# Performance work log

Hardware: AMD Instinct MI355X
Metric: run time of the kernel (lower is better)

## Reference

```python
import jax, jax.numpy as jnp
import numpy as np

B, S, D = 4, 4096, 128

def setup_inputs() -> dict:
    key = jax.random.key(0)
    kq, kk, kv = jax.random.split(key, 3)
    q = jax.random.normal(kq, (B, S, D), dtype=jnp.float32)
    k = jax.random.normal(kk, (B, S, D), dtype=jnp.float32)
    v = jax.random.normal(kv, (B, S, D), dtype=jnp.float32)
    return {"q": q, "k": k, "v": v}

def reference(q, k, v):
    d_model = q.shape[-1]
    scale = 1.0 / jnp.sqrt(jnp.asarray(d_model, q.dtype))
    # [B, S, S] scores
    scores = jnp.einsum('bqd,bkd->bqk', q, k) * scale
    s = q.shape[1]
    causal = jnp.tril(jnp.ones((s, s), dtype=bool))
    neg_inf = jnp.asarray(-jnp.inf, scores.dtype)
    scores = jnp.where(causal[None, :, :], scores, neg_inf)
    attn = jax.nn.softmax(scores, axis=-1)
    return jnp.einsum('bqk,bkd->bqd', attn, v)
```

## Files before the change

### kernel.cpp

```cpp
#include <hip/hip_runtime.h>


#define B_   4
#define S_   4096
#define D_   128
#define BN   64
#define NT_  64
#define QT_  32
#define NCHB 119
#define BLOB_SHORTS 16384
#define MASKVAL (-1.0e30f)
#define DEFER_THR 8.0f

typedef __attribute__((ext_vector_type(8))) short bf16x8;
typedef __attribute__((ext_vector_type(4))) float f32x4;

__device__ __host__ __forceinline__ constexpr int chunks_of(int t) { return (2 * t + 11) / 10; }
constexpr int nchb_calc() { int s = 0; for (int t = 0; t < QT_; ++t) s += chunks_of(t); return s; }
static_assert(nchb_calc() == NCHB, "chunk count mismatch");

__device__ __forceinline__ short f2bf(float x) {
    unsigned u = __builtin_bit_cast(unsigned, x);
    unsigned r = (u + 0x7fffu + ((u >> 16) & 1u)) >> 16;
    return (short)r;
}
__device__ __forceinline__ float ex2(float x) { return __builtin_amdgcn_exp2f(x); }
__device__ __forceinline__ unsigned cvtpk(float lo, float hi) {
    unsigned r;
    asm("v_cvt_pk_bf16_f32 %0, %1, %2" : "=v"(r) : "v"(lo), "v"(hi));
    return r;
}
__device__ __forceinline__ void gl_lds16(const short* g, short* l) {
    __builtin_amdgcn_global_load_lds(
        (const __attribute__((address_space(1))) unsigned int*)g,
        (__attribute__((address_space(3))) unsigned int*)l, 16, 0, 0);
}

__global__ __launch_bounds__(256) void prep(const float* __restrict__ Qg,
                                            const float* __restrict__ Kg,
                                            const float* __restrict__ Vg,
                                            short* __restrict__ Qbf,
                                            short* __restrict__ KV)
{
    __shared__ short vt[64][40];
    const int id  = blockIdx.x;
    const int tid = threadIdx.x;
    const float SC = 0.12751740f;

    if (id < 1024) {
        const int b = id & 3, tile = (id >> 2) & 63, q4 = id >> 8;
        const int n = q4 * 16 + (tid >> 4);
        const int G = tid & 15;
        const size_t rowoff = ((size_t)b * S_ + (size_t)tile * 64 + n) * D_ + G * 8;
        short* blob = KV + (size_t)(b * NT_ + tile) * BLOB_SHORTS;
        {
            float4 a = *reinterpret_cast<const float4*>(Qg + rowoff);
            float4 c = *reinterpret_cast<const float4*>(Qg + rowoff + 4);
            bf16x8 v;
            v[0] = f2bf(a.x * SC); v[1] = f2bf(a.y * SC); v[2] = f2bf(a.z * SC); v[3] = f2bf(a.w * SC);
            v[4] = f2bf(c.x * SC); v[5] = f2bf(c.y * SC); v[6] = f2bf(c.z * SC); v[7] = f2bf(c.w * SC);
            *reinterpret_cast<bf16x8*>(Qbf + rowoff) = v;
        }
        {
            float4 a = *reinterpret_cast<const float4*>(Kg + rowoff);
            float4 c = *reinterpret_cast<const float4*>(Kg + rowoff + 4);
            bf16x8 v;
            v[0] = f2bf(a.x); v[1] = f2bf(a.y); v[2] = f2bf(a.z); v[3] = f2bf(a.w);
            v[4] = f2bf(c.x); v[5] = f2bf(c.y); v[6] = f2bf(c.z); v[7] = f2bf(c.w);
            const int p = (G & 8) | ((G & 7) ^ (n & 7));
            *reinterpret_cast<bf16x8*>(blob + n * 128 + p * 8) = v;
        }
    } else {
        const int u = id - 1024;
        const int b = u & 3, tile = (u >> 2) & 63, dq = u >> 8;
        short* blob = KV + (size_t)(b * NT_ + tile) * BLOB_SHORTS;
        {
            const int n = tid >> 2, c8 = tid & 3;
            const size_t off = ((size_t)b * S_ + (size_t)tile * 64 + n) * D_ + dq * 32 + c8 * 8;
            float4 a = *reinterpret_cast<const float4*>(Vg + off);
            float4 c = *reinterpret_cast<const float4*>(Vg + off + 4);
            bf16x8 v;
            v[0] = f2bf(a.x); v[1] = f2bf(a.y); v[2] = f2bf(a.z); v[3] = f2bf(a.w);
            v[4] = f2bf(c.x); v[5] = f2bf(c.y); v[6] = f2bf(c.z); v[7] = f2bf(c.w);
            *reinterpret_cast<bf16x8*>(&vt[n][c8 * 8]) = v;
        }
        __syncthreads();
        {
            const int dl = tid >> 3, G = tid & 7;
            const int d  = dq * 32 + dl;
            bf16x8 g;
#pragma unroll
            for (int i = 0; i < 8; ++i) g[i] = vt[G * 8 + i][dl];
            const int p = G ^ (d & 7);
            *reinterpret_cast<bf16x8*>(blob + 8192 + d * 64 + p * 8) = g;
        }
    }
}

template<bool SPLIT>
__global__ __launch_bounds__(512, 4) void fa_fwd(const short* __restrict__ Qbf,
                                                 const short* __restrict__ KV,
                                                 float* __restrict__ Og,
                                                 unsigned* __restrict__ Op,
                                                 float* __restrict__ Ml)
{
    __shared__ short lkv[2][BLOB_SHORTS];
    __shared__ unsigned pbuf[8][256];

    const int tid  = threadIdx.x;
    const int wv   = tid >> 6;
    const int lane = tid & 63;
    const int m    = lane & 15;
    const int quad = lane >> 4;
    const int m7   = m & 7;

    int batch, t, lo, hi, chunk_id;
    {
        const int id = blockIdx.x;
        batch = id & 3;
        int u = id >> 2;
        if (SPLIT) {
            int tt = QT_ - 1, base = 0, rt;
            for (;;) { rt = chunks_of(tt); if (u < base + rt) break; base += rt; --tt; }
            t = tt;
            const int r  = u - base;
            const int nk = 2 * t + 2;
            lo = r * nk / rt;
            hi = (r + 1) * nk / rt;
            chunk_id = batch * NCHB + u;
        } else {
            t  = QT_ - 1 - u;
            lo = 0; hi = 2 * t + 2; chunk_id = 0;
        }
        if (lo >= hi) return;
    }

    bf16x8 qf[4];
    {
        const short* qp = Qbf + ((size_t)batch * S_ + (size_t)t * 128 + wv * 16 + m) * D_ + quad * 8;
#pragma unroll
        for (int c = 0; c < 4; ++c)
            qf[c] = *reinterpret_cast<const bf16x8*>(qp + c * 32);
    }

    f32x4 acc[8];
#pragma unroll
    for (int i = 0; i < 8; ++i) acc[i] = (f32x4){0.f, 0.f, 0.f, 0.f};
    float mrun = MASKVAL, lrun = 0.f;

    const size_t tilebase = (size_t)batch * NT_ * BLOB_SHORTS;
    const int qtop = t * 128 + wv * 16 + 15;
#define STAGE(KT, BUF) do {                                                   \
        const short* g_ = KV + tilebase + (size_t)(KT) * BLOB_SHORTS + tid * 8;\
        short* l_ = (BUF) + tid * 8;                                          \
        _Pragma("unroll")                                                     \
        for (int c_ = 0; c_ < 4; ++c_)                                        \
            gl_lds16(g_ + c_ * 4096, l_ + c_ * 4096);                         \
    } while (0)

    STAGE(lo, lkv[0]);

    for (int kt = lo; kt < hi; ++kt) {
        const short* cur = lkv[(kt - lo) & 1];
        short* nxt = lkv[(kt - lo + 1) & 1];
        __syncthreads();
        if (kt + 1 < hi) STAGE(kt + 1, nxt);

        if (kt * 64 > qtop) continue;

        const short* lk = cur;
        const short* lv = cur + 8192;

        f32x4 st[4];
#pragma unroll
        for (int nt = 0; nt < 4; ++nt) st[nt] = (f32x4){0.f, 0.f, 0.f, 0.f};
        __builtin_amdgcn_s_setprio(1);
#pragma unroll
        for (int c = 0; c < 4; ++c) {
            const int p = ((c >> 1) * 8) | ((((c & 1) * 4) | quad) ^ m7);
#pragma unroll
            for (int nt = 0; nt < 4; ++nt) {
                bf16x8 kf = *reinterpret_cast<const bf16x8*>(lk + nt * 2048 + m * 128 + p * 8);
                st[nt] = __builtin_amdgcn_mfma_f32_16x16x32_bf16(kf, qf[c], st[nt], 0, 0, 0);
            }
        }
        __builtin_amdgcn_s_setprio(0);

        if (kt >= 2 * t) {
            const int kbase = (kt - 2 * t) * 64;
            const int qloc  = wv * 16 + m;
#pragma unroll
            for (int nt = 0; nt < 4; ++nt)
#pragma unroll
                for (int r = 0; r < 4; ++r)
                    if (kbase + nt * 16 + quad * 4 + r > qloc) st[nt][r] = MASKVAL;
        }

        float t0 = fmaxf(fmaxf(st[0][0], st[0][1]), fmaxf(st[0][2], st[0][3]));
        float t1 = fmaxf(fmaxf(st[1][0], st[1][1]), fmaxf(st[1][2], st[1][3]));
        float t2 = fmaxf(fmaxf(st[2][0], st[2][1]), fmaxf(st[2][2], st[2][3]));
        float t3 = fmaxf(fmaxf(st[3][0], st[3][1]), fmaxf(st[3][2], st[3][3]));
        float mx = fmaxf(fmaxf(t0, t1), fmaxf(t2, t3));
        if (__any(mx - mrun > DEFER_THR)) {
            float mw = fmaxf(mx, __shfl_xor(mx, 16));
            mw = fmaxf(mw, __shfl_xor(mw, 32));
            const float mnew = fmaxf(mrun, mw);
            const float al   = ex2(mrun - mnew);
            mrun = mnew;
            lrun *= al;
#pragma unroll
            for (int r = 0; r < 4; ++r) {
                float alq = __shfl(al, quad * 4 + r);
#pragma unroll
                for (int ct = 0; ct < 8; ++ct) acc[ct][r] *= alq;
            }
        }
        float sum = 0.f;
#pragma unroll
        for (int nt = 0; nt < 4; ++nt)
#pragma unroll
            for (int r = 0; r < 4; ++r) {
                float pv = ex2(st[nt][r] - mrun);
                st[nt][r] = pv;
                sum += pv;
            }
        lrun += sum;

        {
            unsigned* pb = &pbuf[wv][0];
            const int swz = (m & 3) << 2;
#pragma unroll
            for (int ks = 0; ks < 2; ++ks) {
#pragma unroll
                for (int h = 0; h < 2; ++h) {
                    const int nt = 2 * ks + h;
                    uint2 w;
                    w.x = cvtpk(st[nt][0], st[nt][1]);
                    w.y = cvtpk(st[nt][2], st[nt][3]);
                    *reinterpret_cast<uint2*>(pb + m * 16 + ((h * 8 + quad * 2) ^ swz)) = w;
                }
                uint4 wi = *reinterpret_cast<const uint4*>(pb + m * 16 + ((quad * 4) ^ swz));
                bf16x8 pf = __builtin_bit_cast(bf16x8, wi);
                const int p = (ks * 4 + quad) ^ m7;
                __builtin_amdgcn_s_setprio(1);
#pragma unroll
                for (int ct = 0; ct < 8; ++ct) {
                    bf16x8 vf = *reinterpret_cast<const bf16x8*>(lv + ct * 1024 + m * 64 + p * 8);
                    acc[ct] = __builtin_amdgcn_mfma_f32_16x16x32_bf16(pf, vf, acc[ct], 0, 0, 0);
                }
                __builtin_amdgcn_s_setprio(0);
            }
        }
    }
#undef STAGE

    lrun += __shfl_xor(lrun, 16);
    lrun += __shfl_xor(lrun, 32);

    const int row0 = wv * 16 + quad * 4;
    if (SPLIT) {
        unsigned* ob = Op + (size_t)chunk_id * (128 * 64);
#pragma unroll
        for (int r = 0; r < 4; ++r) {
            uint4 w;
            w.x = cvtpk(acc[0][r], acc[1][r]);
            w.y = cvtpk(acc[2][r], acc[3][r]);
            w.z = cvtpk(acc[4][r], acc[5][r]);
            w.w = cvtpk(acc[6][r], acc[7][r]);
            *reinterpret_cast<uint4*>(ob + (row0 + r) * 64 + m * 4) = w;
        }
        if (lane < 16) {
            float* mlb = Ml + (size_t)chunk_id * (128 * 2) + (wv * 16 + lane) * 2;
            mlb[0] = mrun;
            mlb[1] = lrun;
        }
    } else {
        const float inv = 1.0f / lrun;
        const size_t obase = ((size_t)batch * S_ + (size_t)t * 128 + row0) * D_;
#pragma unroll
        for (int r = 0; r < 4; ++r) {
            float invq = __shfl(inv, quad * 4 + r);
#pragma unroll
            for (int ct = 0; ct < 8; ++ct)
                Og[obase + (size_t)r * D_ + ct * 16 + m] = acc[ct][r] * invq;
        }
    }
}

__global__ __launch_bounds__(256) void fa_merge(const unsigned* __restrict__ Op,
                                                const float* __restrict__ Ml,
                                                float* __restrict__ Og)
{
    const int x   = blockIdx.x;
    const int btq = x >> 4;
    const int oct = x & 15;
    const int t   = btq & (QT_ - 1);
    const int b   = btq >> 5;
    const int rt  = chunks_of(t);
    int base = 0;
    for (int tt = QT_ - 1; tt > t; --tt) base += chunks_of(tt);
    const int cbase = b * NCHB + base;
    const int row = oct * 8 + (threadIdx.x >> 5);
    const int g   = threadIdx.x & 31;

    float mr_[7], lr_[7];
    float mg = MASKVAL;
#pragma unroll
    for (int r = 0; r < 7; ++r)
        if (r < rt) {
            float2 ml2 = *reinterpret_cast<const float2*>(
                Ml + (size_t)(cbase + r) * (128 * 2) + row * 2);
            mr_[r] = ml2.x;
            lr_[r] = ml2.y;
            mg = fmaxf(mg, mr_[r]);
        }
    float l = 0.f;
    float a0 = 0.f, a1 = 0.f, a2 = 0.f, a3 = 0.f;
#pragma unroll
    for (int r = 0; r < 7; ++r)
        if (r < rt) {
            float w = ex2(mr_[r] - mg);
            l += lr_[r] * w;
            uint2 pk = *reinterpret_cast<const uint2*>(
                Op + (size_t)(cbase + r) * (128 * 64) + row * 64 + g * 2);
            a0 += w * __builtin_bit_cast(float, pk.x << 16);
            a1 += w * __builtin_bit_cast(float, pk.x & 0xffff0000u);
            a2 += w * __builtin_bit_cast(float, pk.y << 16);
            a3 += w * __builtin_bit_cast(float, pk.y & 0xffff0000u);
        }
    const float inv = 1.0f / l;
    float* og = Og + (size_t)btq * (128 * D_) + row * D_;
    const int d0 = 64 * (g & 1) + (g >> 1);
    og[d0]      = a0 * inv;
    og[d0 + 16] = a1 * inv;
    og[d0 + 32] = a2 * inv;
    og[d0 + 48] = a3 * inv;
}

extern "C" void kernel_launch(void* const* d_in, const int* in_sizes, int n_in,
                              void* d_out, int out_size, void* d_ws, size_t ws_size,
                              hipStream_t stream) {
    const float* q = (const float*)d_in[0];
    const float* k = (const float*)d_in[1];
    const float* v = (const float*)d_in[2];
    float* o = (float*)d_out;

    const size_t QBF_BYTES = (size_t)B_ * S_ * D_ * 2;
    const size_t KV_BYTES  = (size_t)B_ * NT_ * BLOB_SHORTS * 2;
    const size_t PREFIX    = QBF_BYTES + KV_BYTES;
    const int    NCH       = B_ * NCHB;
    const size_t O_BYTES   = (size_t)NCH * 128 * 64 * 4;
    const size_t ML_BYTES  = (size_t)NCH * 128 * 2 * 4;
    const size_t NEEDED    = PREFIX + O_BYTES + ML_BYTES;

    char* ws = (char*)d_ws;
    short* Qbf = (short*)ws;
    short* KV  = (short*)(ws + QBF_BYTES);

    prep<<<dim3(2048), 256, 0, stream>>>(q, k, v, Qbf, KV);

    if (ws_size >= NEEDED) {
        unsigned* Op = (unsigned*)(ws + PREFIX);
        float* Ml = (float*)(ws + PREFIX + O_BYTES);
        fa_fwd<true><<<dim3(NCH), 512, 0, stream>>>(Qbf, KV, nullptr, Op, Ml);
        fa_merge<<<dim3(B_ * QT_ * 16), 256, 0, stream>>>(Op, Ml, o);
    } else {
        fa_fwd<false><<<dim3(B_ * QT_), 512, 0, stream>>>(Qbf, KV, o, nullptr, nullptr);
    }
}
```

Before: 112.7 us.

## Give each wave two 16-row query tiles and halve block size to 256 threads

Each wavefront now handles 32 query rows as two 16-row halves, reusing every K and V fragment read from LDS for two MFMAs. The block shrinks from 8 to 4 waves, with the K/V staging loop doubled to cover the same tile. This halves LDS read traffic per MFMA but doubles accumulator and score register use per thread and cuts waves per block, which may lower occupancy and latency hiding.

Result: no change. 113.0 us (+0.3%).

```diff
diff --git a/kernel.cpp b/kernel.cpp
--- a/kernel.cpp
+++ b/kernel.cpp
@@ -98,14 +98,14 @@
 }
 
 template<bool SPLIT>
-__global__ __launch_bounds__(512, 4) void fa_fwd(const short* __restrict__ Qbf,
+__global__ __launch_bounds__(256, 2) void fa_fwd(const short* __restrict__ Qbf,
                                                  const short* __restrict__ KV,
                                                  float* __restrict__ Og,
                                                  unsigned* __restrict__ Op,
                                                  float* __restrict__ Ml)
 {
     __shared__ short lkv[2][BLOB_SHORTS];
-    __shared__ unsigned pbuf[8][256];
+    __shared__ unsigned pbuf[4][512];
 
     const int tid  = threadIdx.x;
     const int wv   = tid >> 6;
@@ -135,27 +135,31 @@
         if (lo >= hi) return;
     }
 
-    bf16x8 qf[4];
-    {
-        const short* qp = Qbf + ((size_t)batch * S_ + (size_t)t * 128 + wv * 16 + m) * D_ + quad * 8;
+    bf16x8 qf[2][4];
+#pragma unroll
+    for (int qh = 0; qh < 2; ++qh) {
+        const short* qp = Qbf + ((size_t)batch * S_ + (size_t)t * 128 + wv * 32 + qh * 16 + m) * D_ + quad * 8;
 #pragma unroll
         for (int c = 0; c < 4; ++c)
-            qf[c] = *reinterpret_cast<const bf16x8*>(qp + c * 32);
-    }
-
-    f32x4 acc[8];
-#pragma unroll
-    for (int i = 0; i < 8; ++i) acc[i] = (f32x4){0.f, 0.f, 0.f, 0.f};
-    float mrun = MASKVAL, lrun = 0.f;
+            qf[qh][c] = *reinterpret_cast<const bf16x8*>(qp + c * 32);
+    }
+
+    f32x4 acc[2][8];
+#pragma unroll
+    for (int qh = 0; qh < 2; ++qh)
+#pragma unroll
+        for (int i = 0; i < 8; ++i) acc[qh][i] = (f32x4){0.f, 0.f, 0.f, 0.f};
+    float mrun[2] = {MASKVAL, MASKVAL};
+    float lrun[2] = {0.f, 0.f};
 
     const size_t tilebase = (size_t)batch * NT_ * BLOB_SHORTS;
-    const int qtop = t * 128 + wv * 16 + 15;
+    const int qtop = t * 128 + wv * 32 + 31;
 #define STAGE(KT, BUF) do {                                                   \
         const short* g_ = KV + tilebase + (size_t)(KT) * BLOB_SHORTS + tid * 8;\
         short* l_ = (BUF) + tid * 8;                                          \
         _Pragma("unroll")                                                     \
-        for (int c_ = 0; c_ < 4; ++c_)                                        \
-            gl_lds16(g_ + c_ * 4096, l_ + c_ * 4096);                         \
+        for (int c_ = 0; c_ < 8; ++c_)                                        \
+            gl_lds16(g_ + c_ * 2048, l_ + c_ * 2048);                         \
     } while (0)
 
     STAGE(lo, lkv[0]);
@@ -171,9 +175,11 @@
         const short* lk = cur;
         const short* lv = cur + 8192;
 
-        f32x4 st[4];
-#pragma unroll
-        for (int nt = 0; nt < 4; ++nt) st[nt] = (f32x4){0.f, 0.f, 0.f, 0.f};
+        f32x4 st[2][4];
+#pragma unroll
+        for (int qh = 0; qh < 2; ++qh)
+#pragma unroll
+            for (int nt = 0; nt < 4; ++nt) st[qh][nt] = (f32x4){0.f, 0.f, 0.f, 0.f};
         __builtin_amdgcn_s_setprio(1);
 #pragma unroll
         for (int c = 0; c < 4; ++c) {
@@ -181,72 +187,85 @@
 #pragma unroll
             for (int nt = 0; nt < 4; ++nt) {
                 bf16x8 kf = *reinterpret_cast<const bf16x8*>(lk + nt * 2048 + m * 128 + p * 8);
-                st[nt] = __builtin_amdgcn_mfma_f32_16x16x32_bf16(kf, qf[c], st[nt], 0, 0, 0);
+                st[0][nt] = __builtin_amdgcn_mfma_f32_16x16x32_bf16(kf, qf[0][c], st[0][nt], 0, 0, 0);
+                st[1][nt] = __builtin_amdgcn_mfma_f32_16x16x32_bf16(kf, qf[1][c], st[1][nt], 0, 0, 0);
             }
         }
         __builtin_amdgcn_s_setprio(0);
 
         if (kt >= 2 * t) {
             const int kbase = (kt - 2 * t) * 64;
-            const int qloc  = wv * 16 + m;
+#pragma unroll
+            for (int qh = 0; qh < 2; ++qh) {
+                const int qloc = wv * 32 + qh * 16 + m;
+#pragma unroll
+                for (int nt = 0; nt < 4; ++nt)
+#pragma unroll
+                    for (int r = 0; r < 4; ++r)
+                        if (kbase + nt * 16 + quad * 4 + r > qloc) st[qh][nt][r] = MASKVAL;
+            }
+        }
+
+#pragma unroll
+        for (int qh = 0; qh < 2; ++qh) {
+            float t0 = fmaxf(fmaxf(st[qh][0][0], st[qh][0][1]), fmaxf(st[qh][0][2], st[qh][0][3]));
+            float t1 = fmaxf(fmaxf(st[qh][1][0], st[qh][1][1]), fmaxf(st[qh][1][2], st[qh][1][3]));
+            float t2 = fmaxf(fmaxf(st[qh][2][0], st[qh][2][1]), fmaxf(st[qh][2][2], st[qh][2][3]));
+            float t3 = fmaxf(fmaxf(st[qh][3][0], st[qh][3][1]), fmaxf(st[qh][3][2], st[qh][3][3]));
+            float mx = fmaxf(fmaxf(t0, t1), fmaxf(t2, t3));
+            if (__any(mx - mrun[qh] > DEFER_THR)) {
+                float mw = fmaxf(mx, __shfl_xor(mx, 16));
+                mw = fmaxf(mw, __shfl_xor(mw, 32));
+                const float mnew = fmaxf(mrun[qh], mw);
+                const float al   = ex2(mrun[qh] - mnew);
+                mrun[qh] = mnew;
+                lrun[qh] *= al;
+#pragma unroll
+                for (int r = 0; r < 4; ++r) {
+                    float alq = __shfl(al, quad * 4 + r);
+#pragma unroll
+                    for (int ct = 0; ct < 8; ++ct) acc[qh][ct][r] *= alq;
+                }
+            }
+            float sum = 0.f;
 #pragma unroll
             for (int nt = 0; nt < 4; ++nt)
 #pragma unroll
-                for (int r = 0; r < 4; ++r)
-                    if (kbase + nt * 16 + quad * 4 + r > qloc) st[nt][r] = MASKVAL;
-        }
-
-        float t0 = fmaxf(fmaxf(st[0][0], st[0][1]), fmaxf(st[0][2], st[0][3]));
-        float t1 = fmaxf(fmaxf(st[1][0], st[1][1]), fmaxf(st[1][2], st[1][3]));
-        float t2 = fmaxf(fmaxf(st[2][0], st[2][1]), fmaxf(st[2][2], st[2][3]));
-        float t3 = fmaxf(fmaxf(st[3][0], st[3][1]), fmaxf(st[3][2], st[3][3]));
-        float mx = fmaxf(fmaxf(t0, t1), fmaxf(t2, t3));
-        if (__any(mx - mrun > DEFER_THR)) {
-            float mw = fmaxf(mx, __shfl_xor(mx, 16));
-            mw = fmaxf(mw, __shfl_xor(mw, 32));
-            const float mnew = fmaxf(mrun, mw);
-            const float al   = ex2(mrun - mnew);
-            mrun = mnew;
-            lrun *= al;
-#pragma unroll
-            for (int r = 0; r < 4; ++r) {
-                float alq = __shfl(al, quad * 4 + r);
-#pragma unroll
-                for (int ct = 0; ct < 8; ++ct) acc[ct][r] *= alq;
-            }
-        }
-        float sum = 0.f;
-#pragma unroll
-        for (int nt = 0; nt < 4; ++nt)
-#pragma unroll
-            for (int r = 0; r < 4; ++r) {
-                float pv = ex2(st[nt][r] - mrun);
-                st[nt][r] = pv;
-                sum += pv;
-            }
-        lrun += sum;
+                for (int r = 0; r < 4; ++r) {
+                    float pv = ex2(st[qh][nt][r] - mrun[qh]);
+                    st[qh][nt][r] = pv;
+                    sum += pv;
+                }
+            lrun[qh] += sum;
+        }
 
         {
-            unsigned* pb = &pbuf[wv][0];
             const int swz = (m & 3) << 2;
 #pragma unroll
             for (int ks = 0; ks < 2; ++ks) {
 #pragma unroll
-                for (int h = 0; h < 2; ++h) {
-                    const int nt = 2 * ks + h;
-                    uint2 w;
-                    w.x = cvtpk(st[nt][0], st[nt][1]);
-                    w.y = cvtpk(st[nt][2], st[nt][3]);
-                    *reinterpret_cast<uint2*>(pb + m * 16 + ((h * 8 + quad * 2) ^ swz)) = w;
+                for (int qh = 0; qh < 2; ++qh) {
+                    unsigned* pb = &pbuf[wv][qh * 256];
+#pragma unroll
+                    for (int h = 0; h < 2; ++h) {
+                        const int nt = 2 * ks + h;
+                        uint2 w;
+                        w.x = cvtpk(st[qh][nt][0], st[qh][nt][1]);
+                        w.y = cvtpk(st[qh][nt][2], st[qh][nt][3]);
+                        *reinterpret_cast<uint2*>(pb + m * 16 + ((h * 8 + quad * 2) ^ swz)) = w;
+                    }
                 }
-                uint4 wi = *reinterpret_cast<const uint4*>(pb + m * 16 + ((quad * 4) ^ swz));
-                bf16x8 pf = __builtin_bit_cast(bf16x8, wi);
+                uint4 wi0 = *reinterpret_cast<const uint4*>(&pbuf[wv][0]   + m * 16 + ((quad * 4) ^ swz));
+                uint4 wi1 = *reinterpret_cast<const uint4*>(&pbuf[wv][256] + m * 16 + ((quad * 4) ^ swz));
+                bf16x8 pf0 = __builtin_bit_cast(bf16x8, wi0);
+                bf16x8 pf1 = __builtin_bit_cast(bf16x8, wi1);
                 const int p = (ks * 4 + quad) ^ m7;
                 __builtin_amdgcn_s_setprio(1);
 #pragma unroll
                 for (int ct = 0; ct < 8; ++ct) {
                     bf16x8 vf = *reinterpret_cast<const bf16x8*>(lv + ct * 1024 + m * 64 + p * 8);
-                    acc[ct] = __builtin_amdgcn_mfma_f32_16x16x32_bf16(pf, vf, acc[ct], 0, 0, 0);
+                    acc[0][ct] = __builtin_amdgcn_mfma_f32_16x16x32_bf16(pf0, vf, acc[0][ct], 0, 0, 0);
+                    acc[1][ct] = __builtin_amdgcn_mfma_f32_16x16x32_bf16(pf1, vf, acc[1][ct], 0, 0, 0);
                 }
                 __builtin_amdgcn_s_setprio(0);
             }
@@ -254,35 +273,48 @@
     }
 #undef STAGE
 
-    lrun += __shfl_xor(lrun, 16);
-    lrun += __shfl_xor(lrun, 32);
-
-    const int row0 = wv * 16 + quad * 4;
+#pragma unroll
+    for (int qh = 0; qh < 2; ++qh) {
+        lrun[qh] += __shfl_xor(lrun[qh], 16);
+        lrun[qh] += __shfl_xor(lrun[qh], 32);
+    }
+
     if (SPLIT) {
         unsigned* ob = Op + (size_t)chunk_id * (128 * 64);
 #pragma unroll
-        for (int r = 0; r < 4; ++r) {
-            uint4 w;
-            w.x = cvtpk(acc[0][r], acc[1][r]);
-            w.y = cvtpk(acc[2][r], acc[3][r]);
-            w.z = cvtpk(acc[4][r], acc[5][r]);
-            w.w = cvtpk(acc[6][r], acc[7][r]);
-            *reinterpret_cast<uint4*>(ob + (row0 + r) * 64 + m * 4) = w;
+        for (int qh = 0; qh < 2; ++qh) {
+            const int row0 = wv * 32 + qh * 16 + quad * 4;
+#pragma unroll
+            for (int r = 0; r < 4; ++r) {
+                uint4 w;
+                w.x = cvtpk(acc[qh][0][r], acc[qh][1][r]);
+                w.y = cvtpk(acc[qh][2][r], acc[qh][3][r]);
+                w.z = cvtpk(acc[qh][4][r], acc[qh][5][r]);
+                w.w = cvtpk(acc[qh][6][r], acc[qh][7][r]);
+                *reinterpret_cast<uint4*>(ob + (row0 + r) * 64 + m * 4) = w;
+            }
         }
         if (lane < 16) {
-            float* mlb = Ml + (size_t)chunk_id * (128 * 2) + (wv * 16 + lane) * 2;
-            mlb[0] = mrun;
-            mlb[1] = lrun;
+#pragma unroll
+            for (int qh = 0; qh < 2; ++qh) {
+                float* mlb = Ml + (size_t)chunk_id * (128 * 2) + (wv * 32 + qh * 16 + lane) * 2;
+                mlb[0] = mrun[qh];
+                mlb[1] = lrun[qh];
+            }
         }
     } else {
-        const float inv = 1.0f / lrun;
-        const size_t obase = ((size_t)batch * S_ + (size_t)t * 128 + row0) * D_;
-#pragma unroll
-        for (int r = 0; r < 4; ++r) {
-            float invq = __shfl(inv, quad * 4 + r);
-#pragma unroll
-            for (int ct = 0; ct < 8; ++ct)
-                Og[obase + (size_t)r * D_ + ct * 16 + m] = acc[ct][r] * invq;
+#pragma unroll
+        for (int qh = 0; qh < 2; ++qh) {
+            const float inv = 1.0f / lrun[qh];
+            const int row0 = wv * 32 + qh * 16 + quad * 4;
+            const size_t obase = ((size_t)batch * S_ + (size_t)t * 128 + row0) * D_;
+#pragma unroll
+            for (int r = 0; r < 4; ++r) {
+                float invq = __shfl(inv, quad * 4 + r);
+#pragma unroll
+                for (int ct = 0; ct < 8; ++ct)
+                    Og[obase + (size_t)r * D_ + ct * 16 + m] = acc[qh][ct][r] * invq;
+            }
         }
     }
 }
@@ -362,9 +394,9 @@
     if (ws_size >= NEEDED) {
         unsigned* Op = (unsigned*)(ws + PREFIX);
         float* Ml = (float*)(ws + PREFIX + O_BYTES);
-        fa_fwd<true><<<dim3(NCH), 512, 0, stream>>>(Qbf, KV, nullptr, Op, Ml);
+        fa_fwd<true><<<dim3(NCH), 256, 0, stream>>>(Qbf, KV, nullptr, Op, Ml);
         fa_merge<<<dim3(B_ * QT_ * 16), 256, 0, stream>>>(Op, Ml, o);
     } else {
-        fa_fwd<false><<<dim3(B_ * QT_), 512, 0, stream>>>(Qbf, KV, o, nullptr, nullptr);
-    }
-}
+        fa_fwd<false><<<dim3(B_ * QT_), 256, 0, stream>>>(Qbf, KV, o, nullptr, nullptr);
+    }
+}
```
